# Optimization experiments

Measured on AMD Instinct MI355X. Metric: run time of the kernel, lower is better.

The kernel has to match this reference:

```python
import jax, jax.numpy as jnp
import numpy as np

N, D, H, HI = 4096, 3, 64, 8
THRE = 0.5
M_PARTICLES = 16.0
USE_MASS = True
EPS = 1e-8


def setup_inputs() -> dict:
    key = jax.random.key(0)
    ks = jax.random.split(key, 10)
    g = lambda k, shape, sc=1.0: (jax.random.normal(k, shape, jnp.float32) * sc)
    return {
        "t": jnp.full((1,), 0.5, jnp.float32),
        "z": g(ks[0], (N, D)),
        "lnw": g(ks[1], (N, 1), 0.1),
        "W1": g(ks[2], (D + 1, H), 1.0 / np.sqrt(D + 1)),
        "b1": jnp.zeros((H,), jnp.float32),
        "Wv": g(ks[3], (H, D), 1.0 / np.sqrt(H)),
        "bv": jnp.zeros((D,), jnp.float32),
        "Wg": g(ks[4], (H, 1), 1.0 / np.sqrt(H)),
        "bg": jnp.zeros((1,), jnp.float32),
        "Wi1": g(ks[5], (HI,)),
        "bi1": g(ks[6], (HI,), 0.1),
        "Wi2": g(ks[7], (HI,), 1.0 / np.sqrt(HI)),
        "bi2": jnp.zeros((1,), jnp.float32),
    }


def reference(t, z, lnw, W1, b1, Wv, bv, Wg, bg, Wi1, bi1, Wi2, bi2):
    n = z.shape[0]
    # ---- f_net: drift v and growth g from concat(z, t) -> tanh MLP ----
    tcol = jnp.broadcast_to(t.reshape(1, 1), (n, 1))
    h = jnp.tanh(jnp.concatenate([z, tcol], axis=1) @ W1 + b1)  # [n, H]
    v = h @ Wv + bv                                              # [n, d]
    grow = h @ Wg + bg                                           # [n, 1]

    # ---- cal_interaction: thresholded pairwise potential force ----
    diff = z[:, None, :] - z[None, :, :]                 # [n, n, d]
    dist = jnp.sqrt(jnp.sum(diff * diff, axis=-1) + EPS)  # [n, n]
    # interaction potential U(r) = Wi2 . tanh(r*Wi1 + bi1) + bi2
    # analytic dU/dr = sum_k Wi2[k] * Wi1[k] * sech^2(r*Wi1[k] + bi1[k])
    pre = dist[..., None] * Wi1 + bi1                    # [n, n, HI]
    dU = jnp.einsum('ijk,k->ij', 1.0 - jnp.tanh(pre) ** 2, Wi1 * Wi2)  # [n, n]
    mask = (dist < THRE).astype(z.dtype) * (1.0 - jnp.eye(n, dtype=z.dtype))
    w = jnp.exp(lnw)                                     # [n, 1] mass weights
    wj = w[:, 0][None, :] if USE_MASS else jnp.ones((1, n), z.dtype)
    # force_i = -(1/m) * sum_j mask * w_j * U'(r_ij) * (z_i - z_j)/r_ij
    coeff = -(mask * wj * dU / dist) / M_PARTICLES       # [n, n]
    net_force = jnp.einsum('ij,ijd->id', coeff, diff)    # [n, d]

    dz_dt = v + net_force
    dlnw_dt = grow
    if USE_MASS:
        dm_dt = (jnp.sum(v * v, axis=1, keepdims=True) + grow ** 2) * w
    else:
        dm_dt = jnp.sum(v * v, axis=1, keepdims=True)
    return (dz_dt, dlnw_dt, dm_dt)
```

## Files before the change

kernel.cpp:

```cpp
#include <hip/hip_runtime.h>
#include <hip/hip_fp16.h>
#include <math.h>

#define NPART 4096
#define HID 64
#define HI 8
#define IPB 16
#define BLOCK (IPB * 64)
#define NUNIT (NPART / 4)
#define CAP 256
#define TBL 256
#define TSCALE ((float)(TBL - 1) / 0.5f)
#define SCAN_THR 0.26f

struct alignas(8) H2x2 { __half2 a, b; };

__global__ __launch_bounds__(BLOCK) void odefunc_kernel(
    const float* __restrict__ t_in,
    const float* __restrict__ z,
    const float* __restrict__ lnw,
    const float* __restrict__ W1,
    const float* __restrict__ b1,
    const float* __restrict__ Wv,
    const float* __restrict__ bv,
    const float* __restrict__ Wg,
    const float* __restrict__ bg,
    const float* __restrict__ Wi1,
    const float* __restrict__ bi1,
    const float* __restrict__ Wi2,
    const float* __restrict__ bi2,
    float* __restrict__ out)
{
    __shared__ H2x2 sX2[NUNIT];
    __shared__ H2x2 sY2[NUNIT];
    __shared__ H2x2 sZ2[NUNIT];
    __shared__ float sT[TBL];
    __shared__ unsigned short lists[IPB][CAP];

    const int tid = threadIdx.x;

    {
        const float4* z4 = (const float4*)z;
        const float4 r0 = z4[3 * tid + 0];
        const float4 r1 = z4[3 * tid + 1];
        const float4 r2 = z4[3 * tid + 2];
        H2x2 hx, hy, hz;
        hx.a = __floats2half2_rn(r0.x, r0.w);
        hx.b = __floats2half2_rn(r1.z, r2.y);
        hy.a = __floats2half2_rn(r0.y, r1.x);
        hy.b = __floats2half2_rn(r1.w, r2.z);
        hz.a = __floats2half2_rn(r0.z, r1.y);
        hz.b = __floats2half2_rn(r2.x, r2.w);
        sX2[tid] = hx;
        sY2[tid] = hy;
        sZ2[tid] = hz;

        if (tid < TBL) {
            const float r = (float)tid * (0.5f / (float)(TBL - 1));
            float acc = 0.f;
            #pragma unroll
            for (int kk = 0; kk < HI; ++kk) {
                const float s = __expf(-2.0f * fmaf(r, Wi1[kk], bi1[kk]));
                const float den = 1.0f + s;
                acc += 4.0f * Wi1[kk] * Wi2[kk] * s *
                       __builtin_amdgcn_rcpf(den * den);
            }
            sT[tid] = acc;
        }
    }
    __syncthreads();

    const int lane = tid & 63;
    const int wid  = tid >> 6;
    const int i    = blockIdx.x * IPB + wid;

    const float zix = z[3 * i + 0];
    const float ziy = z[3 * i + 1];
    const float ziz = z[3 * i + 2];

    float v0, v1, v2, grow;
    {
        const float tval = t_in[0];
        float pre = zix * W1[0 * HID + lane]
                  + ziy * W1[1 * HID + lane]
                  + ziz * W1[2 * HID + lane]
                  + tval * W1[3 * HID + lane]
                  + b1[lane];
        const float e2 = __expf(2.0f * pre);
        const float h = 1.0f - 2.0f * __builtin_amdgcn_rcpf(e2 + 1.0f);
        float pv0 = h * Wv[lane * 3 + 0];
        float pv1 = h * Wv[lane * 3 + 1];
        float pv2 = h * Wv[lane * 3 + 2];
        float pg  = h * Wg[lane];
        #pragma unroll
        for (int s = 1; s < 64; s <<= 1) {
            pv0 += __shfl_xor(pv0, s);
            pv1 += __shfl_xor(pv1, s);
            pv2 += __shfl_xor(pv2, s);
            pg  += __shfl_xor(pg, s);
        }
        v0 = pv0 + bv[0];
        v1 = pv1 + bv[1];
        v2 = pv2 + bv[2];
        grow = pg + bg[0];
    }

    unsigned short* myl = lists[wid];
    int cnt = 0;

    {
        const __half2 hxi = __float2half2_rn(zix);
        const __half2 hyi = __float2half2_rn(ziy);
        const __half2 hzi = __float2half2_rn(ziz);
        for (int tt = 0; tt < NUNIT / 64; ++tt) {
            const int u = tt * 64 + lane;
            const H2x2 xs = sX2[u];
            const H2x2 ys = sY2[u];
            const H2x2 zs = sZ2[u];
            const __half2 dxa = __hsub2(hxi, xs.a);
            const __half2 dya = __hsub2(hyi, ys.a);
            const __half2 dza = __hsub2(hzi, zs.a);
            const __half2 dxb = __hsub2(hxi, xs.b);
            const __half2 dyb = __hsub2(hyi, ys.b);
            const __half2 dzb = __hsub2(hzi, zs.b);
            const __half2 d2a = __hfma2(dxa, dxa, __hfma2(dya, dya, __hmul2(dza, dza)));
            const __half2 d2b = __hfma2(dxb, dxb, __hfma2(dyb, dyb, __hmul2(dzb, dzb)));
            const float m0 = __low2float(d2a), m1 = __high2float(d2a);
            const float m2 = __low2float(d2b), m3 = __high2float(d2b);
            const float m = fminf(fminf(m0, m1), fminf(m2, m3));
            const bool pred = (m < SCAN_THR);
            const unsigned long long bal = __ballot(pred);
            const unsigned int lo = (unsigned int)bal, hi = (unsigned int)(bal >> 32);
            const int pre = __builtin_amdgcn_mbcnt_hi(hi, __builtin_amdgcn_mbcnt_lo(lo, 0u));
            if (pred) myl[cnt + pre] = (unsigned short)u;
            cnt += __popcll(bal);
        }
    }

    float fx = 0.f, fy = 0.f, fz = 0.f;
    {
        const float4* z4 = (const float4*)z;
        const float4* l4 = (const float4*)lnw;
        for (int base = 0; base < cnt; base += 64) {
            const int k = base + lane;
            const bool valid = (k < cnt);
            const int e = valid ? (int)myl[k] : 0;
            const float4 r0 = z4[3 * e + 0];
            const float4 r1 = z4[3 * e + 1];
            const float4 r2 = z4[3 * e + 2];
            const float4 lw = l4[e];
            #pragma unroll
            for (int q = 0; q < 4; ++q) {
                const int j = 4 * e + q;
                const float xj = (q == 0) ? r0.x : (q == 1) ? r0.w : (q == 2) ? r1.z : r2.y;
                const float yj = (q == 0) ? r0.y : (q == 1) ? r1.x : (q == 2) ? r1.w : r2.z;
                const float zj = (q == 0) ? r0.z : (q == 1) ? r1.y : (q == 2) ? r2.x : r2.w;
                const float lj = (q == 0) ? lw.x : (q == 1) ? lw.y : (q == 2) ? lw.z : lw.w;
                const float dx = zix - xj;
                const float dy = ziy - yj;
                const float dz = ziz - zj;
                const float d2 = dx * dx + dy * dy + dz * dz + 1e-8f;
                const float r = __builtin_amdgcn_sqrtf(d2);
                const bool ok = valid && (r < 0.5f) && (j != i);
                const float u = r * TSCALE;
                int i0 = (int)u;
                i0 = i0 > (TBL - 2) ? (TBL - 2) : i0;
                const float fr = u - (float)i0;
                const float t0 = sT[i0], t1 = sT[i0 + 1];
                const float dU = fmaf(fr, t1 - t0, t0);
                const float wj = __expf(lj);
                const float coeff = ok
                    ? (-0.0625f) * wj * dU * __builtin_amdgcn_rcpf(r) : 0.0f;
                fx = fmaf(coeff, dx, fx);
                fy = fmaf(coeff, dy, fy);
                fz = fmaf(coeff, dz, fz);
            }
        }
    }

    #pragma unroll
    for (int s = 1; s < 64; s <<= 1) {
        fx += __shfl_xor(fx, s);
        fy += __shfl_xor(fy, s);
        fz += __shfl_xor(fz, s);
    }

    if (lane == 0) {
        out[i * 3 + 0] = v0 + fx;
        out[i * 3 + 1] = v1 + fy;
        out[i * 3 + 2] = v2 + fz;
        out[NPART * 3 + i] = grow;
        const float wi = __expf(lnw[i]);
        out[NPART * 3 + NPART + i] =
            (v0 * v0 + v1 * v1 + v2 * v2 + grow * grow) * wi;
    }
}

extern "C" void kernel_launch(void* const* d_in, const int* in_sizes, int n_in,
                              void* d_out, int out_size, void* d_ws, size_t ws_size,
                              hipStream_t stream) {
    const float* t_in = (const float*)d_in[0];
    const float* z    = (const float*)d_in[1];
    const float* lnw  = (const float*)d_in[2];
    const float* W1   = (const float*)d_in[3];
    const float* b1   = (const float*)d_in[4];
    const float* Wv   = (const float*)d_in[5];
    const float* bv   = (const float*)d_in[6];
    const float* Wg   = (const float*)d_in[7];
    const float* bg   = (const float*)d_in[8];
    const float* Wi1  = (const float*)d_in[9];
    const float* bi1  = (const float*)d_in[10];
    const float* Wi2  = (const float*)d_in[11];
    const float* bi2  = (const float*)d_in[12];
    (void)bi2;
    float* out = (float*)d_out;

    odefunc_kernel<<<dim3(NPART / IPB), dim3(BLOCK), 0, stream>>>(
        t_in, z, lnw, W1, b1, Wv, bv, Wg, bg, Wi1, bi1, Wi2, bi2, out);
}
```

Measured before the change: 13.47 us.

## Split each particle's neighbor scan across two wavefronts and combine partial forces

Each block now handles 8 particles with 16 waves, so two waves share one particle and each scans half of the candidate units. Partial forces from the second wave go through shared memory and are added by the first wave after a block barrier. This doubles the grid size and shortens each wave's serial scan, and the per-wave list capacity shrinks to match. The cost is that the shared z staging and the table build are repeated across twice as many blocks, plus one extra barrier. The smaller list capacity could overflow on inputs with denser neighborhoods.

```diff
diff --git a/kernel.cpp b/kernel.cpp
--- a/kernel.cpp
+++ b/kernel.cpp
@@ -5,17 +5,19 @@
 #define NPART 4096
 #define HID 64
 #define HI 8
-#define IPB 16
-#define BLOCK (IPB * 64)
+#define PPB 8
+#define WPB 16
+#define BLOCK (WPB * 64)
 #define NUNIT (NPART / 4)
-#define CAP 256
+#define HUNIT (NUNIT / 2)
+#define CAP 144
 #define TBL 256
 #define TSCALE ((float)(TBL - 1) / 0.5f)
 #define SCAN_THR 0.26f
 
 struct alignas(8) H2x2 { __half2 a, b; };
 
-__global__ __launch_bounds__(BLOCK) void odefunc_kernel(
+__global__ __launch_bounds__(BLOCK, 8) void odefunc_kernel(
     const float* __restrict__ t_in,
     const float* __restrict__ z,
     const float* __restrict__ lnw,
@@ -35,7 +37,8 @@
     __shared__ H2x2 sY2[NUNIT];
     __shared__ H2x2 sZ2[NUNIT];
     __shared__ float sT[TBL];
-    __shared__ unsigned short lists[IPB][CAP];
+    __shared__ unsigned short lists[WPB][CAP];
+    __shared__ float pf[PPB][3];
 
     const int tid = threadIdx.x;
 
@@ -72,14 +75,16 @@
 
     const int lane = tid & 63;
     const int wid  = tid >> 6;
-    const int i    = blockIdx.x * IPB + wid;
+    const int pidx = wid & (PPB - 1);
+    const int half = wid >> 3;
+    const int i    = blockIdx.x * PPB + pidx;
 
     const float zix = z[3 * i + 0];
     const float ziy = z[3 * i + 1];
     const float ziz = z[3 * i + 2];
 
-    float v0, v1, v2, grow;
-    {
+    float v0 = 0.f, v1 = 0.f, v2 = 0.f, grow = 0.f;
+    if (half == 0) {
         const float tval = t_in[0];
         float pre = zix * W1[0 * HID + lane]
                   + ziy * W1[1 * HID + lane]
@@ -112,8 +117,10 @@
         const __half2 hxi = __float2half2_rn(zix);
         const __half2 hyi = __float2half2_rn(ziy);
         const __half2 hzi = __float2half2_rn(ziz);
-        for (int tt = 0; tt < NUNIT / 64; ++tt) {
-            const int u = tt * 64 + lane;
+        const int ubase = half * HUNIT;
+        #pragma unroll 2
+        for (int tt = 0; tt < HUNIT / 64; ++tt) {
+            const int u = ubase + tt * 64 + lane;
             const H2x2 xs = sX2[u];
             const H2x2 ys = sY2[u];
             const H2x2 zs = sZ2[u];
@@ -185,10 +192,17 @@
         fz += __shfl_xor(fz, s);
     }
 
-    if (lane == 0) {
-        out[i * 3 + 0] = v0 + fx;
-        out[i * 3 + 1] = v1 + fy;
-        out[i * 3 + 2] = v2 + fz;
+    if (half == 1 && lane == 0) {
+        pf[pidx][0] = fx;
+        pf[pidx][1] = fy;
+        pf[pidx][2] = fz;
+    }
+    __syncthreads();
+
+    if (half == 0 && lane == 0) {
+        out[i * 3 + 0] = v0 + fx + pf[pidx][0];
+        out[i * 3 + 1] = v1 + fy + pf[pidx][1];
+        out[i * 3 + 2] = v2 + fz + pf[pidx][2];
         out[NPART * 3 + i] = grow;
         const float wi = __expf(lnw[i]);
         out[NPART * 3 + NPART + i] =
@@ -215,6 +229,6 @@
     (void)bi2;
     float* out = (float*)d_out;
 
-    odefunc_kernel<<<dim3(NPART / IPB), dim3(BLOCK), 0, stream>>>(
+    odefunc_kernel<<<dim3(NPART / PPB), dim3(BLOCK), 0, stream>>>(
         t_in, z, lnw, W1, b1, Wv, bv, Wg, bg, Wi1, bi1, Wi2, bi2, out);
 }
```

Result: slower. 14.32 us (+6.3%).
